# Kernel tuning notes

Hardware: AMD Instinct MI355X
Metric: run time of the kernel (lower is better)

The kernel has to match this reference:

```python
import jax, jax.numpy as jnp
import numpy as np

HIDDEN_DIM = 512  # H; hidden/encoder feature dim is 2H = 1024


def setup_inputs() -> dict:
    key = jax.random.key(0)
    k1, k2, k3, k4, k5 = jax.random.split(key, 5)
    B, S, D2, H = 16, 4096, 2 * HIDDEN_DIM, HIDDEN_DIM
    hidden = jax.random.normal(k1, (B, D2), dtype=jnp.float32)
    encoder_outputs = jax.random.normal(k2, (B, S, D2), dtype=jnp.float32)
    # nn.Linear(4H, H): weight [H, 4H] in torch; store transposed [4H, H] for x @ W
    W_attn = jax.random.normal(k3, (2 * D2, H), dtype=jnp.float32) * (1.0 / np.sqrt(2 * D2))
    b_attn = jax.random.normal(k4, (H,), dtype=jnp.float32) * 0.01
    # nn.Linear(H, 1, bias=False): weight [1, H] -> vector [H]
    w_v = jax.random.normal(k5, (H,), dtype=jnp.float32) * (1.0 / np.sqrt(H))
    return {"hidden": hidden, "encoder_outputs": encoder_outputs,
            "W_attn": W_attn, "b_attn": b_attn, "w_v": w_v}


def reference(hidden, encoder_outputs, W_attn, b_attn, w_v):
    B, S, D2 = encoder_outputs.shape
    # Broadcast decoder hidden over seq positions and concat with encoder outputs.
    hid = jnp.broadcast_to(hidden[:, None, :], (B, S, D2))
    cat = jnp.concatenate([hid, encoder_outputs], axis=2)        # [B, S, 4H]
    energy = jnp.tanh(cat @ W_attn + b_attn)                      # [B, S, H]
    scores = jnp.einsum('bsh,h->bs', energy, w_v)                 # [B, S]
    attention = jax.nn.softmax(scores, axis=1)                    # [B, S]
    context = jnp.einsum('bs,bsd->bd', attention, encoder_outputs)  # [B, 2H]
    return context
```

## Files before the change

kernel.cpp:

```cpp
#include <hip/hip_runtime.h>
#include <hip/hip_bf16.h>
#include <math.h>

#define HD   512
#define D2   1024
#define SEQ  4096
#define BAT  16
#define BM   64
#define BK   32

typedef _Float16 half8 __attribute__((ext_vector_type(8)));
typedef float    f32x4 __attribute__((ext_vector_type(4)));

typedef __attribute__((address_space(3))) void lds_void_t;
typedef __attribute__((address_space(1))) void glb_void_t;

__global__ void wconv_kernel(const float* __restrict__ W, _Float16* __restrict__ Wt) {
  __shared__ float tile[32][33];
  const int kb = blockIdx.x * 32;
  const int nb = blockIdx.y * 32;
  const int tx = threadIdx.x & 31;
  const int ty = threadIdx.x >> 5;
  #pragma unroll
  for (int i = 0; i < 4; ++i) {
    int kl = ty + i * 8;
    tile[kl][tx] = W[(size_t)(D2 + kb + kl) * HD + nb + tx];
  }
  __syncthreads();
  #pragma unroll
  for (int i = 0; i < 4; ++i) {
    int nl = ty + i * 8;
    Wt[(size_t)(nb + nl) * D2 + kb + tx] = (_Float16)tile[tx][nl];
  }
}

__global__ void hproj_kernel(const float* __restrict__ hidden,
                             const float* __restrict__ W,
                             float* __restrict__ hproj) {
  const int b  = blockIdx.x >> 3;
  const int kc = blockIdx.x & 7;
  const int h  = threadIdx.x;
  float a0 = 0.f, a1 = 0.f;
  #pragma unroll 4
  for (int i = 0; i < 128; ++i) {
    const int d = kc * 128 + i;
    const float hd = hidden[b * D2 + d];
    a0 += hd * W[(size_t)d * HD + h];
    a1 += hd * W[(size_t)d * HD + h + 256];
  }
  atomicAdd(&hproj[b * HD + h], a0);
  atomicAdd(&hproj[b * HD + h + 256], a1);
}

__global__ __launch_bounds__(256, 2) void scores_kernel(
    const float* __restrict__ enc, const _Float16* __restrict__ Wt,
    const float* __restrict__ hproj, const float* __restrict__ b_attn,
    const float* __restrict__ w_v, float* __restrict__ scores)
{
  __shared__ __align__(16) _Float16 As[BM][BK + 8];
  __shared__ __align__(16) _Float16 Bs[HD * BK];

  const int b    = blockIdx.y;
  const int s0   = blockIdx.x * BM;
  const int tid  = threadIdx.x;
  const int lane = tid & 63;
  const int wave = tid >> 6;
  const int strip = wave >> 1;
  const int nhalf = wave & 1;
  const int col  = lane & 15;
  const int quad = lane >> 4;

  const float* encB = enc + ((size_t)b * SEQ + s0) * D2;

  f32x4 acc0[16], acc1[16];
  const f32x4 z = {0.f, 0.f, 0.f, 0.f};
  #pragma unroll
  for (int i = 0; i < 16; ++i) { acc0[i] = z; acc1[i] = z; }

  const int arow = tid >> 2;
  const int akq  = tid & 3;

  for (int kt = 0; kt < D2 / BK; ++kt) {
    __syncthreads();
    {
      const float* src = encB + (size_t)arow * D2 + kt * BK + akq * 8;
      f32x4 v0 = *(const f32x4*)(src);
      f32x4 v1 = *(const f32x4*)(src + 4);
      half8 hv;
      hv[0] = (_Float16)v0[0]; hv[1] = (_Float16)v0[1];
      hv[2] = (_Float16)v0[2]; hv[3] = (_Float16)v0[3];
      hv[4] = (_Float16)v1[0]; hv[5] = (_Float16)v1[1];
      hv[6] = (_Float16)v1[2]; hv[7] = (_Float16)v1[3];
      *(half8*)&As[arow][akq * 8] = hv;
    }
    #pragma unroll
    for (int i = 0; i < 8; ++i) {
      const int c   = i * 256 + tid;
      const int n   = c >> 2;
      const int khs = c & 3;
      const int kg  = khs ^ (n & 3);
      __builtin_amdgcn_global_load_lds(
          (glb_void_t*)((const char*)Wt + (size_t)n * (D2 * 2) + (size_t)kt * 64 + kg * 16),
          (lds_void_t*)((char*)Bs + c * 16), 16, 0, 0);
    }
    __syncthreads();
    half8 a0 = *(const half8*)&As[strip * 32 + col][quad * 8];
    half8 a1 = *(const half8*)&As[strip * 32 + 16 + col][quad * 8];
    #pragma unroll
    for (int nt = 0; nt < 16; ++nt) {
      const int n = nhalf * 256 + nt * 16 + col;
      half8 bf = *(const half8*)((const char*)Bs + n * 64 + ((quad ^ (n & 3)) * 16));
      acc0[nt] = __builtin_amdgcn_mfma_f32_16x16x32_f16(a0, bf, acc0[nt], 0, 0, 0);
      acc1[nt] = __builtin_amdgcn_mfma_f32_16x16x32_f16(a1, bf, acc1[nt], 0, 0, 0);
    }
  }

  float p0[4] = {0.f, 0.f, 0.f, 0.f}, p1[4] = {0.f, 0.f, 0.f, 0.f};
  const float* hp = hproj + b * HD;
  #pragma unroll
  for (int nt = 0; nt < 16; ++nt) {
    const int n = nhalf * 256 + nt * 16 + col;
    const float hb = hp[n] + b_attn[n];
    const float wv = w_v[n];
    #pragma unroll
    for (int r = 0; r < 4; ++r) {
      p0[r] += wv * tanhf(acc0[nt][r] + hb);
      p1[r] += wv * tanhf(acc1[nt][r] + hb);
    }
  }
  #pragma unroll
  for (int off = 8; off >= 1; off >>= 1) {
    #pragma unroll
    for (int r = 0; r < 4; ++r) {
      p0[r] += __shfl_xor(p0[r], off, 64);
      p1[r] += __shfl_xor(p1[r], off, 64);
    }
  }
  if (col == 0) {
    const int m0 = s0 + strip * 32 + quad * 4;
    #pragma unroll
    for (int r = 0; r < 4; ++r) {
      atomicAdd(&scores[b * SEQ + m0 + r], p0[r]);
      atomicAdd(&scores[b * SEQ + m0 + 16 + r], p1[r]);
    }
  }
}

__global__ void softmax_kernel(float* __restrict__ scores) {
  const int b = blockIdx.x;
  float* sc = scores + b * SEQ;
  __shared__ float red[16];
  const int tid = threadIdx.x;
  float loc[16];
  float mx = -1e30f;
  #pragma unroll
  for (int i = 0; i < 16; ++i) { loc[i] = sc[i * 256 + tid]; mx = fmaxf(mx, loc[i]); }
  #pragma unroll
  for (int off = 32; off >= 1; off >>= 1) mx = fmaxf(mx, __shfl_xor(mx, off, 64));
  if ((tid & 63) == 0) red[tid >> 6] = mx;
  __syncthreads();
  mx = fmaxf(fmaxf(red[0], red[1]), fmaxf(red[2], red[3]));
  float sum = 0.f;
  #pragma unroll
  for (int i = 0; i < 16; ++i) { loc[i] = __expf(loc[i] - mx); sum += loc[i]; }
  #pragma unroll
  for (int off = 32; off >= 1; off >>= 1) sum += __shfl_xor(sum, off, 64);
  if ((tid & 63) == 0) red[8 + (tid >> 6)] = sum;
  __syncthreads();
  sum = red[8] + red[9] + red[10] + red[11];
  const float inv = 1.0f / sum;
  #pragma unroll
  for (int i = 0; i < 16; ++i) sc[i * 256 + tid] = loc[i] * inv;
}

__global__ void context_kernel(const float* __restrict__ attn,
                               const float* __restrict__ enc,
                               float* __restrict__ out) {
  const int b  = blockIdx.y;
  const int s0 = blockIdx.x * 128;
  const int tid = threadIdx.x;
  f32x4 acc = {0.f, 0.f, 0.f, 0.f};
  const float* encB = enc + ((size_t)b * SEQ + s0) * D2;
  const float* at = attn + b * SEQ + s0;
  for (int i = 0; i < 128; ++i) {
    const float a = at[i];
    f32x4 v = *(const f32x4*)(encB + (size_t)i * D2 + tid * 4);
    acc += v * a;
  }
  float* o = out + b * D2 + tid * 4;
  atomicAdd(o + 0, acc[0]);
  atomicAdd(o + 1, acc[1]);
  atomicAdd(o + 2, acc[2]);
  atomicAdd(o + 3, acc[3]);
}

extern "C" void kernel_launch(void* const* d_in, const int* in_sizes, int n_in,
                              void* d_out, int out_size, void* d_ws, size_t ws_size,
                              hipStream_t stream) {
  (void)in_sizes; (void)n_in; (void)ws_size;
  const float* hidden = (const float*)d_in[0];
  const float* enc    = (const float*)d_in[1];
  const float* W      = (const float*)d_in[2];
  const float* b_attn = (const float*)d_in[3];
  const float* w_v    = (const float*)d_in[4];
  float* out = (float*)d_out;

  char* ws = (char*)d_ws;
  _Float16* Wt  = (_Float16*)ws;
  float* hproj  = (float*)(ws + (1 << 20));
  float* scores = (float*)(ws + (1 << 20) + 32768);

  hipMemsetAsync(d_out, 0, (size_t)out_size * sizeof(float), stream);
  hipMemsetAsync(hproj, 0, BAT * HD * sizeof(float), stream);
  hipMemsetAsync(scores, 0, (size_t)BAT * SEQ * sizeof(float), stream);

  wconv_kernel  <<<dim3(32, 16),        256, 0, stream>>>(W, Wt);
  hproj_kernel  <<<dim3(128),           256, 0, stream>>>(hidden, W, hproj);
  scores_kernel <<<dim3(SEQ / BM, BAT), 256, 0, stream>>>(enc, Wt, hproj, b_attn, w_v, scores);
  softmax_kernel<<<dim3(BAT),           256, 0, stream>>>(scores);
  context_kernel<<<dim3(SEQ / 128, BAT),256, 0, stream>>>(scores, enc, out);
}
```

Before: 549.3 us.

## Double-buffer scores GEMM, split N across blocks, pre-swizzle weights, fast tanh

Result: faster. 491.8 us (-10.5%).

```diff
diff --git a/kernel.cpp b/kernel.cpp
--- a/kernel.cpp
+++ b/kernel.cpp
@@ -7,30 +7,35 @@
 #define SEQ  4096
 #define BAT  16
 #define BM   64
+#define BN   256
 #define BK   32
 
 typedef _Float16 half8 __attribute__((ext_vector_type(8)));
 typedef float    f32x4 __attribute__((ext_vector_type(4)));
-
 typedef __attribute__((address_space(3))) void lds_void_t;
 typedef __attribute__((address_space(1))) void glb_void_t;
 
-__global__ void wconv_kernel(const float* __restrict__ W, _Float16* __restrict__ Wt) {
-  __shared__ float tile[32][33];
-  const int kb = blockIdx.x * 32;
-  const int nb = blockIdx.y * 32;
-  const int tx = threadIdx.x & 31;
-  const int ty = threadIdx.x >> 5;
-  #pragma unroll
-  for (int i = 0; i < 4; ++i) {
-    int kl = ty + i * 8;
-    tile[kl][tx] = W[(size_t)(D2 + kb + kl) * HD + nb + tx];
-  }
-  __syncthreads();
-  #pragma unroll
-  for (int i = 0; i < 4; ++i) {
-    int nl = ty + i * 8;
-    Wt[(size_t)(nb + nl) * D2 + kb + tx] = (_Float16)tile[tx][nl];
+__global__ void wconv_kernel(const float* __restrict__ W, _Float16* __restrict__ WtS) {
+  __shared__ float tile[32][17];
+  const int kt  = blockIdx.x;
+  const int nbg = blockIdx.y;
+  const int nh  = nbg >> 4, nbl = nbg & 15;
+  const int t   = threadIdx.x;
+  {
+    const int n16 = t & 15, kk = t >> 4;
+    #pragma unroll
+    for (int i = 0; i < 2; ++i) {
+      const int k = kk + i * 16;
+      tile[k][n16] = W[(size_t)(D2 + kt * 32 + k) * HD + nh * 256 + nbl * 16 + n16];
+    }
+  }
+  __syncthreads();
+  if (t < 64) {
+    const int kc = t >> 4, nlo = t & 15;
+    half8 h;
+    #pragma unroll
+    for (int j = 0; j < 8; ++j) h[j] = (_Float16)tile[kc * 8 + j][nlo];
+    *(half8*)(WtS + ((size_t)(kt * 2 + nh) * 1024 + nbl * 64 + kc * 16 + nlo) * 8) = h;
   }
 }
 
@@ -52,80 +57,112 @@
   atomicAdd(&hproj[b * HD + h + 256], a1);
 }
 
-__global__ __launch_bounds__(256, 2) void scores_kernel(
-    const float* __restrict__ enc, const _Float16* __restrict__ Wt,
+__global__ __launch_bounds__(256, 4) void scores_kernel(
+    const float* __restrict__ enc, const _Float16* __restrict__ WtS,
     const float* __restrict__ hproj, const float* __restrict__ b_attn,
     const float* __restrict__ w_v, float* __restrict__ scores)
 {
-  __shared__ __align__(16) _Float16 As[BM][BK + 8];
-  __shared__ __align__(16) _Float16 Bs[HD * BK];
-
-  const int b    = blockIdx.y;
-  const int s0   = blockIdx.x * BM;
-  const int tid  = threadIdx.x;
-  const int lane = tid & 63;
-  const int wave = tid >> 6;
-  const int strip = wave >> 1;
-  const int nhalf = wave & 1;
-  const int col  = lane & 15;
-  const int quad = lane >> 4;
+  __shared__ __align__(16) _Float16 As[2][BM * BK];
+  __shared__ __align__(16) _Float16 Bs[2][BN * BK];
+
+  const int s0  = blockIdx.x * BM;
+  const int nh  = blockIdx.y;
+  const int b   = blockIdx.z;
+  const int tid = threadIdx.x, lane = tid & 63, w = tid >> 6;
+  const int col = lane & 15, quad = lane >> 4;
+  const int strip = w >> 1, nq2 = w & 1;
 
   const float* encB = enc + ((size_t)b * SEQ + s0) * D2;
-
-  f32x4 acc0[16], acc1[16];
+  const _Float16* WtB = WtS + (size_t)nh * 1024 * 8;
+
+  const int arow = tid >> 2, akc = tid & 3;
+  const float* aSrcBase = encB + (size_t)arow * D2 + akc * 8;
+  const int aDstOff = (akc * 64 + (arow ^ (akc << 2))) * 8;
+  const int a0off = (quad * 64 + ((strip * 32 + col)      ^ (quad << 2))) * 8;
+  const int a1off = (quad * 64 + ((strip * 32 + 16 + col) ^ (quad << 2))) * 8;
+
+  f32x4 acc0[8], acc1[8];
   const f32x4 z = {0.f, 0.f, 0.f, 0.f};
   #pragma unroll
-  for (int i = 0; i < 16; ++i) { acc0[i] = z; acc1[i] = z; }
-
-  const int arow = tid >> 2;
-  const int akq  = tid & 3;
-
-  for (int kt = 0; kt < D2 / BK; ++kt) {
-    __syncthreads();
-    {
-      const float* src = encB + (size_t)arow * D2 + kt * BK + akq * 8;
-      f32x4 v0 = *(const f32x4*)(src);
-      f32x4 v1 = *(const f32x4*)(src + 4);
-      half8 hv;
-      hv[0] = (_Float16)v0[0]; hv[1] = (_Float16)v0[1];
-      hv[2] = (_Float16)v0[2]; hv[3] = (_Float16)v0[3];
-      hv[4] = (_Float16)v1[0]; hv[5] = (_Float16)v1[1];
-      hv[6] = (_Float16)v1[2]; hv[7] = (_Float16)v1[3];
-      *(half8*)&As[arow][akq * 8] = hv;
-    }
-    #pragma unroll
-    for (int i = 0; i < 8; ++i) {
-      const int c   = i * 256 + tid;
-      const int n   = c >> 2;
-      const int khs = c & 3;
-      const int kg  = khs ^ (n & 3);
+  for (int i = 0; i < 8; ++i) { acc0[i] = z; acc1[i] = z; }
+
+  f32x4 Ra0, Ra1, Rb0, Rb1;
+
+  auto loadA = [&](int kt, f32x4& v0, f32x4& v1) {
+    const float* p = aSrcBase + kt * BK;
+    v0 = *(const f32x4*)p;
+    v1 = *(const f32x4*)(p + 4);
+  };
+  auto storeA = [&](int buf, const f32x4& v0, const f32x4& v1) {
+    half8 h;
+    h[0] = (_Float16)v0[0]; h[1] = (_Float16)v0[1];
+    h[2] = (_Float16)v0[2]; h[3] = (_Float16)v0[3];
+    h[4] = (_Float16)v1[0]; h[5] = (_Float16)v1[1];
+    h[6] = (_Float16)v1[2]; h[7] = (_Float16)v1[3];
+    *(half8*)&As[buf][aDstOff] = h;
+  };
+  auto issueB = [&](int kt, int buf) {
+    #pragma unroll
+    for (int i = 0; i < 4; ++i) {
+      const int c = i * 256 + tid;
       __builtin_amdgcn_global_load_lds(
-          (glb_void_t*)((const char*)Wt + (size_t)n * (D2 * 2) + (size_t)kt * 64 + kg * 16),
-          (lds_void_t*)((char*)Bs + c * 16), 16, 0, 0);
-    }
-    __syncthreads();
-    half8 a0 = *(const half8*)&As[strip * 32 + col][quad * 8];
-    half8 a1 = *(const half8*)&As[strip * 32 + 16 + col][quad * 8];
-    #pragma unroll
-    for (int nt = 0; nt < 16; ++nt) {
-      const int n = nhalf * 256 + nt * 16 + col;
-      half8 bf = *(const half8*)((const char*)Bs + n * 64 + ((quad ^ (n & 3)) * 16));
+          (glb_void_t*)(WtB + (size_t)kt * 16384 + c * 8),
+          (lds_void_t*)((char*)&Bs[buf][0] + c * 16), 16, 0, 0);
+    }
+  };
+  auto compute = [&](int buf) {
+    half8 a0 = *(const half8*)&As[buf][a0off];
+    half8 a1 = *(const half8*)&As[buf][a1off];
+    #pragma unroll
+    for (int nt = 0; nt < 8; ++nt) {
+      const int nbl_local = nq2 * 8 + nt;
+      half8 bf = *(const half8*)&Bs[buf][(nbl_local * 64 + quad * 16 + col) * 8];
       acc0[nt] = __builtin_amdgcn_mfma_f32_16x16x32_f16(a0, bf, acc0[nt], 0, 0, 0);
       acc1[nt] = __builtin_amdgcn_mfma_f32_16x16x32_f16(a1, bf, acc1[nt], 0, 0, 0);
     }
+  };
+
+  loadA(0, Ra0, Ra1);
+  storeA(0, Ra0, Ra1);
+  issueB(0, 0);
+  loadA(1, Rb0, Rb1);
+  __syncthreads();
+
+  #pragma unroll 2
+  for (int kt = 0; kt < 32; ++kt) {
+    const int cur = kt & 1, nxt = cur ^ 1;
+    if (kt + 1 < 32) issueB(kt + 1, nxt);
+    if (kt + 2 < 32) {
+      if (kt & 1) loadA(kt + 2, Rb0, Rb1);
+      else        loadA(kt + 2, Ra0, Ra1);
+    }
+    compute(cur);
+    if (kt + 1 < 32) {
+      if (kt & 1) storeA(nxt, Ra0, Ra1);
+      else        storeA(nxt, Rb0, Rb1);
+    }
+    __syncthreads();
   }
 
   float p0[4] = {0.f, 0.f, 0.f, 0.f}, p1[4] = {0.f, 0.f, 0.f, 0.f};
-  const float* hp = hproj + b * HD;
-  #pragma unroll
-  for (int nt = 0; nt < 16; ++nt) {
-    const int n = nhalf * 256 + nt * 16 + col;
-    const float hb = hp[n] + b_attn[n];
-    const float wv = w_v[n];
+  const float* hp = hproj + b * HD + nh * 256;
+  #pragma unroll
+  for (int nt = 0; nt < 8; ++nt) {
+    const int nl = nq2 * 128 + nt * 16 + col;
+    const float hb = hp[nl] + b_attn[nh * 256 + nl];
+    const float wv = w_v[nh * 256 + nl];
     #pragma unroll
     for (int r = 0; r < 4; ++r) {
-      p0[r] += wv * tanhf(acc0[nt][r] + hb);
-      p1[r] += wv * tanhf(acc1[nt][r] + hb);
+      {
+        float x = fminf(fmaxf(acc0[nt][r] + hb, -15.f), 15.f);
+        float ex = __expf(2.f * x);
+        p0[r] += wv * __fdividef(ex - 1.f, ex + 1.f);
+      }
+      {
+        float x = fminf(fmaxf(acc1[nt][r] + hb, -15.f), 15.f);
+        float ex = __expf(2.f * x);
+        p1[r] += wv * __fdividef(ex - 1.f, ex + 1.f);
+      }
     }
   }
   #pragma unroll
@@ -173,20 +210,21 @@
   for (int i = 0; i < 16; ++i) sc[i * 256 + tid] = loc[i] * inv;
 }
 
-__global__ void context_kernel(const float* __restrict__ attn,
-                               const float* __restrict__ enc,
-                               float* __restrict__ out) {
+__global__ __launch_bounds__(256) void context_kernel(const float* __restrict__ attn,
+                                                      const float* __restrict__ enc,
+                                                      float* __restrict__ out) {
   const int b  = blockIdx.y;
-  const int s0 = blockIdx.x * 128;
+  const int s0 = blockIdx.x * 64;
   const int tid = threadIdx.x;
-  f32x4 acc = {0.f, 0.f, 0.f, 0.f};
-  const float* encB = enc + ((size_t)b * SEQ + s0) * D2;
-  const float* at = attn + b * SEQ + s0;
-  for (int i = 0; i < 128; ++i) {
-    const float a = at[i];
-    f32x4 v = *(const f32x4*)(encB + (size_t)i * D2 + tid * 4);
-    acc += v * a;
-  }
+  const float* encB = enc + ((size_t)b * SEQ + s0) * D2 + tid * 4;
+  const float* at   = attn + b * SEQ + s0;
+  f32x4 acc0 = {0.f, 0.f, 0.f, 0.f}, acc1 = {0.f, 0.f, 0.f, 0.f};
+  #pragma unroll 8
+  for (int i = 0; i < 64; i += 2) {
+    acc0 += at[i]     * *(const f32x4*)(encB + (size_t)i * D2);
+    acc1 += at[i + 1] * *(const f32x4*)(encB + (size_t)(i + 1) * D2);
+  }
+  f32x4 acc = acc0 + acc1;
   float* o = out + b * D2 + tid * 4;
   atomicAdd(o + 0, acc[0]);
   atomicAdd(o + 1, acc[1]);
@@ -206,7 +244,7 @@
   float* out = (float*)d_out;
 
   char* ws = (char*)d_ws;
-  _Float16* Wt  = (_Float16*)ws;
+  _Float16* WtS = (_Float16*)ws;
   float* hproj  = (float*)(ws + (1 << 20));
   float* scores = (float*)(ws + (1 << 20) + 32768);
 
@@ -214,9 +252,9 @@
   hipMemsetAsync(hproj, 0, BAT * HD * sizeof(float), stream);
   hipMemsetAsync(scores, 0, (size_t)BAT * SEQ * sizeof(float), stream);
 
-  wconv_kernel  <<<dim3(32, 16),        256, 0, stream>>>(W, Wt);
-  hproj_kernel  <<<dim3(128),           256, 0, stream>>>(hidden, W, hproj);
-  scores_kernel <<<dim3(SEQ / BM, BAT), 256, 0, stream>>>(enc, Wt, hproj, b_attn, w_v, scores);
-  softmax_kernel<<<dim3(BAT),           256, 0, stream>>>(scores);
-  context_kernel<<<dim3(SEQ / 128, BAT),256, 0, stream>>>(scores, enc, out);
-}
+  wconv_kernel  <<<dim3(32, 32),            256, 0, stream>>>(W, WtS);
+  hproj_kernel  <<<dim3(128),               256, 0, stream>>>(hidden, W, hproj);
+  scores_kernel <<<dim3(SEQ / BM, 2, BAT),  256, 0, stream>>>(enc, WtS, hproj, b_attn, w_v, scores);
+  softmax_kernel<<<dim3(BAT),               256, 0, stream>>>(scores);
+  context_kernel<<<dim3(SEQ / 64, BAT),     256, 0, stream>>>(scores, enc, out);
+}
```
